# Kernel optimization log

Hardware: AMD Instinct MI355X
Metric: run time of the kernel (lower is better)

The kernel has to match this reference:

```python
import jax, jax.numpy as jnp
import numpy as np

B, N = 32, 25200          # batch, anchors (YOLOX @ 1280, strides 8/16/32)
NUM_CLASSES = 80
CH = 5 + NUM_CLASSES
CONF_THRE = 0.7
NMS_THRE = 0.45
TOPK = 512                # fixed pre-/post-NMS candidate budget (jit-static)
CLASS_OFFSET = 4096.0     # class-offset trick from the torch code


def setup_inputs() -> dict:
    key = jax.random.key(0)
    pred = jax.random.uniform(key, (B, N, CH), dtype=jnp.float32)
    # put box coords in pixel scale so IoU/NMS behaves realistically
    pred = pred.at[..., :4].multiply(640.0)
    return {"prediction": pred}


def _pairwise_iou(boxes):
    # boxes: [K, 4] xyxy -> iou: [K, K] (same math as torchvision.ops.nms)
    x1, y1, x2, y2 = boxes[:, 0], boxes[:, 1], boxes[:, 2], boxes[:, 3]
    area = (x2 - x1) * (y2 - y1)
    iw = jnp.clip(jnp.minimum(x2[:, None], x2[None, :]) - jnp.maximum(x1[:, None], x1[None, :]), 0.0)
    ih = jnp.clip(jnp.minimum(y2[:, None], y2[None, :]) - jnp.maximum(y1[:, None], y1[None, :]), 0.0)
    inter = iw * ih
    return inter / (area[:, None] + area[None, :] - inter)


def _greedy_nms(boxes, valid, iou_thre):
    # boxes are pre-sorted by descending score; greedy suppression identical to torchvision NMS
    iou = _pairwise_iou(boxes)  # [K, K]
    idx = jnp.arange(boxes.shape[0])

    def body(i, keep):
        suppress = (iou[i] > iou_thre) & (idx > i) & keep[i]
        return keep & ~suppress

    return jax.lax.fori_loop(0, boxes.shape[0], body, valid)


def _per_image(pred):
    # pred: [N, 5+C]
    cx, cy, w, h = pred[:, 0], pred[:, 1], pred[:, 2], pred[:, 3]
    hw, hh = w * 0.5, h * 0.5
    boxes = jnp.stack([cx - hw, cy - hh, cx + hw, cy + hh], axis=1)  # [N, 4] xyxy

    cls_scores = pred[:, 5:5 + NUM_CLASSES]
    class_conf = jnp.max(cls_scores, axis=1)
    class_pred = jnp.argmax(cls_scores, axis=1)
    conf = pred[:, 4] * class_conf                      # obj * class score
    valid = conf >= CONF_THRE

    # confidence filter + sort-by-score via fixed-size top-k (invalids ranked last)
    rank = jnp.where(valid, conf, -1.0)
    _, order = jax.lax.top_k(rank, TOPK)                # [TOPK], descending score
    b = boxes[order]
    c = conf[order]
    cl = class_pred[order]
    v = valid[order]

    nms_boxes = b + cl.astype(b.dtype)[:, None] * CLASS_OFFSET
    keep = _greedy_nms(nms_boxes, v, NMS_THRE)          # [TOPK] bool

    det = jnp.concatenate([b, c[:, None], cl.astype(jnp.float32)[:, None]], axis=1)  # [TOPK, 6]
    det = det * jax.lax.stop_gradient(keep.astype(det.dtype))[:, None]
    return det, keep


def reference(prediction):
    # returns padded detections [B, TOPK, 6] (x1,y1,x2,y2,conf,cls) and keep mask [B, TOPK]
    det, keep = jax.vmap(_per_image)(prediction)
    return det, keep
```

## Files before the change

kernel.cpp:

```cpp
#include <hip/hip_runtime.h>
#include <stdint.h>

#define BATCH 32
#define NANCH 25200
#define CH 85
#define NCLS 80
#define TOPK 512
#define CONF_THRE 0.7f
#define NMS_THRE 0.45f
#define CLS_OFF 4096.0f
#define NCHUNK 25
#define CHUNK 1008

typedef unsigned long long u64;
typedef unsigned int u32;

#define OFF_CONF  0
#define OFF_HIST  3225600
#define OFF_NMS   4044800
#define OFF_DET   4372480
#define OFF_VALID 4765696
#define OFF_MASK  4767744

__global__ __launch_bounds__(256) void scan_kernel(const float* __restrict__ pred,
                                                   u32* __restrict__ conf32) {
    const int tid = threadIdx.x;
    const int lane = tid & 63;
    const int wv = tid >> 6;
    const int g = lane >> 4;
    const int l = lane & 15;
    const int a = blockIdx.x * 16 + wv * 4 + g;
    const size_t base = (size_t)a * CH;

    float m = -1.0f, obj = 0.0f;
    {
        const float4 q = *(const float4*)(pred + base + (l << 2));
        const int p = l << 2;
        if (p + 0 >= 5) m = fmaxf(m, q.x); else if (p + 0 == 4) obj = q.x;
        if (p + 1 >= 5) m = fmaxf(m, q.y); else if (p + 1 == 4) obj = q.y;
        if (p + 2 >= 5) m = fmaxf(m, q.z); else if (p + 2 == 4) obj = q.z;
        if (p + 3 >= 5) m = fmaxf(m, q.w); else if (p + 3 == 4) obj = q.w;
    }
    if (l < 5) {
        const float4 q = *(const float4*)(pred + base + 64 + (l << 2));
        m = fmaxf(fmaxf(m, fmaxf(q.x, q.y)), fmaxf(q.z, q.w));
    } else if (l == 5) {
        m = fmaxf(m, pred[base + 84]);
    }
    #pragma unroll
    for (int off = 1; off < 16; off <<= 1) m = fmaxf(m, __shfl_xor(m, off));
    const float ob = __shfl(obj, (lane & 48) + 1);
    const float conf = ob * m;
    if (l == 0)
        conf32[a] = (conf >= CONF_THRE) ? __float_as_uint(conf) : 0u;
}

__global__ __launch_bounds__(256) void hist_kernel(const u32* __restrict__ conf32,
                                                   u32* __restrict__ histG) {
    __shared__ u32 h[256];
    const int img = blockIdx.x, chunk = blockIdx.y, tid = threadIdx.x;
    h[tid] = 0u;
    __syncthreads();
    const u32* cd = conf32 + (size_t)img * NANCH + chunk * CHUNK;
    for (int i = tid; i < CHUNK; i += 256) {
        const u32 c = cd[i];
        if (c) atomicAdd(&h[(c >> 15) & 255u], 1u);
    }
    __syncthreads();
    histG[((size_t)img * NCHUNK + chunk) * 256 + tid] = h[tid];
}

__global__ __launch_bounds__(1024) void select_kernel(const float* __restrict__ pred,
                                                      const u32* __restrict__ conf32,
                                                      const u32* __restrict__ histG,
                                                      float* __restrict__ nmsG,
                                                      float* __restrict__ detG,
                                                      u64* __restrict__ validG) {
    __shared__ u64 sbuf[1024];
    __shared__ u64 sorted[1024];
    __shared__ u32 hist[256];
    __shared__ u32 wtot[4];
    __shared__ u32 s_cnt, s_pivot;
    __shared__ unsigned char val[TOPK];

    const int img = blockIdx.x;
    const int tid = threadIdx.x;
    const int lane = tid & 63;
    const int wv = tid >> 6;

    if (tid == 0) { s_cnt = 0u; s_pivot = 0u; }
    if (tid < 256) {
        const u32* hsrc = histG + (size_t)img * (NCHUNK * 256) + tid;
        u32 s0 = 0;
        #pragma unroll
        for (int c = 0; c < NCHUNK; ++c) s0 += hsrc[c * 256];
        hist[tid] = s0;
    }
    __syncthreads();
    u32 v = 0, s = 0;
    if (tid < 256) {
        v = hist[tid]; s = v;
        #pragma unroll
        for (int off = 1; off < 64; off <<= 1) {
            const u32 t = __shfl_down(s, off);
            if (lane + off < 64) s += t;
        }
        if (lane == 0) wtot[wv] = s;
    }
    __syncthreads();
    if (tid < 256) {
        u32 add = 0;
        for (int w2 = wv + 1; w2 < 4; ++w2) add += wtot[w2];
        const u32 sfull = s + add;
        const u32 snext = sfull - v;
        if (sfull >= TOPK && snext < TOPK) s_pivot = (u32)tid;
    }
    __syncthreads();
    const u32 T = 0x3F000000u | (s_pivot << 15);

    const u32* cd = conf32 + (size_t)img * NANCH;
    for (int i = tid; i < NANCH; i += 1024) {
        const u32 c = cd[i];
        if (c >= T) {
            const u32 pos = atomicAdd(&s_cnt, 1u);
            if (pos < 1024u)
                sbuf[pos] = ((u64)c << 32) | (u64)(0xFFFFFFFFu - (u32)i);
        }
    }
    __syncthreads();
    const u32 mc = (s_cnt > 1024u) ? 1024u : s_cnt;

    sorted[tid] = 0ull;
    u32 rank = 0; u64 my = 0ull;
    if (tid < (int)mc) {
        my = sbuf[tid];
        for (u32 i = 0; i < mc; ++i) rank += (sbuf[i] > my) ? 1u : 0u;
    }
    __syncthreads();
    if (tid < (int)mc && rank < 1024u) sorted[rank] = my;
    __syncthreads();

    float* nb_ = nmsG + (size_t)img * (5 * TOPK);
    float* dt_ = detG + (size_t)img * (6 * TOPK);
    for (int r = wv; r < TOPK; r += 16) {
        const u64 key = sorted[r];
        const float conf = __uint_as_float((u32)(key >> 32));
        const bool okrow = conf >= CONF_THRE;
        float x1 = 0.f, y1 = 0.f, x2 = 0.f, y2 = 0.f, clsf = 0.f;
        if (okrow) {
            const u32 anchor = 0xFFFFFFFFu - (u32)(key & 0xFFFFFFFFull);
            const float* row = pred + ((size_t)img * NANCH + anchor) * CH;
            float vv = row[5 + lane];
            int ci = lane;
            if (lane < 16) {
                const float v2 = row[69 + lane];
                if (v2 > vv) { vv = v2; ci = 64 + lane; }
            }
            #pragma unroll
            for (int off = 32; off > 0; off >>= 1) {
                const float ov = __shfl_xor(vv, off);
                const int oi = __shfl_xor(ci, off);
                if (ov > vv || (ov == vv && oi < ci)) { vv = ov; ci = oi; }
            }
            const float cx = row[0], cy = row[1], w = row[2], h = row[3];
            const float hw = w * 0.5f, hh = h * 0.5f;
            x1 = cx - hw; y1 = cy - hh; x2 = cx + hw; y2 = cy + hh;
            clsf = (float)ci;
        }
        if (lane == 0) {
            const float off = clsf * CLS_OFF;
            const float X1 = x1 + off, Y1 = y1 + off, X2 = x2 + off, Y2 = y2 + off;
            nb_[0 * TOPK + r] = X1; nb_[1 * TOPK + r] = Y1;
            nb_[2 * TOPK + r] = X2; nb_[3 * TOPK + r] = Y2;
            nb_[4 * TOPK + r] = (X2 - X1) * (Y2 - Y1);
            dt_[r * 6 + 0] = x1; dt_[r * 6 + 1] = y1;
            dt_[r * 6 + 2] = x2; dt_[r * 6 + 3] = y2;
            dt_[r * 6 + 4] = okrow ? conf : 0.0f;
            dt_[r * 6 + 5] = clsf;
            val[r] = okrow ? 1 : 0;
        }
    }
    __syncthreads();

    if (tid < TOPK) {
        const u64 vb = __ballot(val[tid] != 0);
        if (lane == 0) validG[img * 8 + wv] = vb;
    }
}

__global__ __launch_bounds__(256) void iou_kernel(const float* __restrict__ nmsG,
                                                  u64* __restrict__ maskG) {
    __shared__ float bx1[TOPK], by1[TOPK], bx2[TOPK], by2[TOPK], bar[TOPK];
    const int img = blockIdx.x;
    const int slab = blockIdx.y;
    const int tid = threadIdx.x;
    const int lane = tid & 63;
    const float* nb_ = nmsG + (size_t)img * (5 * TOPK);
    for (int i = tid; i < TOPK; i += 256) {
        bx1[i] = nb_[i];            by1[i] = nb_[TOPK + i];
        bx2[i] = nb_[2 * TOPK + i]; by2[i] = nb_[3 * TOPK + i];
        bar[i] = nb_[4 * TOPK + i];
    }
    __syncthreads();
    const int q0 = slab * (16 * TOPK);
    for (int q = q0 + tid; q < q0 + 16 * TOPK; q += 256) {
        const int i = q >> 9;
        const int j = q & (TOPK - 1);
        bool sup = false;
        if (j > i) {
            const float xx1 = fmaxf(bx1[i], bx1[j]);
            const float yy1 = fmaxf(by1[i], by1[j]);
            const float xx2 = fminf(bx2[i], bx2[j]);
            const float yy2 = fminf(by2[i], by2[j]);
            const float iw = fmaxf(xx2 - xx1, 0.0f);
            const float ih = fmaxf(yy2 - yy1, 0.0f);
            const float inter = iw * ih;
            const float uni = bar[i] + bar[j] - inter;
            const float iou = inter / uni;
            sup = iou > NMS_THRE;
        }
        const u64 bm = __ballot(sup);
        if (lane == 0) maskG[(size_t)img * 4096 + (q >> 6)] = bm;
    }
}

__global__ __launch_bounds__(256) void greedy_kernel(const u64* __restrict__ maskG,
                                                     const u64* __restrict__ validG,
                                                     const float* __restrict__ detG,
                                                     float* __restrict__ out) {
    __shared__ u64 m[TOPK * 8];
    __shared__ u64 kw8[8];
    const int img = blockIdx.x;
    const int tid = threadIdx.x;
    const int lane = tid & 63;
    const int wv = tid >> 6;
    const u64* mg = maskG + (size_t)img * 4096;
    for (int i = tid; i < 4096; i += 256) m[i] = mg[i];
    __syncthreads();

    if (wv == 0) {
        const bool ld = lane < 8;
        u64 kw = ld ? validG[img * 8 + lane] : 0ull;
        u64 p0 = ld ? m[0 * 8 + lane] : 0ull;
        u64 p1 = ld ? m[1 * 8 + lane] : 0ull;
        u64 p2 = ld ? m[2 * 8 + lane] : 0ull;
        u64 p3 = ld ? m[3 * 8 + lane] : 0ull;
        for (int i = 0; i < TOPK; i += 4) {
            {
                const u64 w = __shfl(kw, i >> 6);
                const u64 bit = (w >> (i & 63)) & 1ull;
                kw &= ~(p0 & (0ull - bit));
                p0 = (ld && i + 4 < TOPK) ? m[(i + 4) * 8 + lane] : 0ull;
            }
            {
                const u64 w = __shfl(kw, (i + 1) >> 6);
                const u64 bit = (w >> ((i + 1) & 63)) & 1ull;
                kw &= ~(p1 & (0ull - bit));
                p1 = (ld && i + 5 < TOPK) ? m[(i + 5) * 8 + lane] : 0ull;
            }
            {
                const u64 w = __shfl(kw, (i + 2) >> 6);
                const u64 bit = (w >> ((i + 2) & 63)) & 1ull;
                kw &= ~(p2 & (0ull - bit));
                p2 = (ld && i + 6 < TOPK) ? m[(i + 6) * 8 + lane] : 0ull;
            }
            {
                const u64 w = __shfl(kw, (i + 3) >> 6);
                const u64 bit = (w >> ((i + 3) & 63)) & 1ull;
                kw &= ~(p3 & (0ull - bit));
                p3 = (ld && i + 7 < TOPK) ? m[(i + 7) * 8 + lane] : 0ull;
            }
        }
        if (ld) kw8[lane] = kw;
    }
    __syncthreads();

    const float* dt_ = detG + (size_t)img * (6 * TOPK);
    float* det_out = out + (size_t)img * (TOPK * 6);
    float* keep_out = out + (size_t)BATCH * TOPK * 6 + (size_t)img * TOPK;
    for (int idx = tid; idx < TOPK * 6; idx += 256) {
        const int r = idx / 6;
        const float kf = ((kw8[r >> 6] >> (r & 63)) & 1ull) ? 1.0f : 0.0f;
        det_out[idx] = dt_[idx] * kf;
    }
    for (int r = tid; r < TOPK; r += 256) {
        keep_out[r] = ((kw8[r >> 6] >> (r & 63)) & 1ull) ? 1.0f : 0.0f;
    }
}

extern "C" void kernel_launch(void* const* d_in, const int* in_sizes, int n_in,
                              void* d_out, int out_size, void* d_ws, size_t ws_size,
                              hipStream_t stream) {
    const float* pred = (const float*)d_in[0];
    float* out = (float*)d_out;
    char* ws = (char*)d_ws;
    u32* conf32 = (u32*)(ws + OFF_CONF);
    u32* histG = (u32*)(ws + OFF_HIST);
    float* nmsG = (float*)(ws + OFF_NMS);
    float* detG = (float*)(ws + OFF_DET);
    u64* validG = (u64*)(ws + OFF_VALID);
    u64* maskG = (u64*)(ws + OFF_MASK);

    scan_kernel<<<(BATCH * NANCH) / 16, 256, 0, stream>>>(pred, conf32);
    dim3 g2(BATCH, NCHUNK);
    hist_kernel<<<g2, 256, 0, stream>>>(conf32, histG);
    select_kernel<<<BATCH, 1024, 0, stream>>>(pred, conf32, histG, nmsG, detG, validG);
    dim3 g4(BATCH, 32);
    iou_kernel<<<g4, 256, 0, stream>>>(nmsG, maskG);
    greedy_kernel<<<BATCH, 256, 0, stream>>>(maskG, validG, detG, out);
}
```

Measured before the change: 484.2 us.

## Fuse histogram into scan and merge select, IoU and greedy into one kernel

Builds the per-image score histogram with global atomics inside the scan kernel, after a small zeroing kernel, so the separate histogram pass is gone. The select, IoU-mask and greedy NMS stages are merged into one 1024-thread block per image that keeps boxes, the suppression mask and detections in shared memory instead of writing them to global memory. The goal is fewer launches and less global round-tripping. In exchange, the IoU matrix is computed by only 32 blocks rather than 1024, and global atomics may contend on the histogram bins.

```diff
diff --git a/kernel.cpp b/kernel.cpp
--- a/kernel.cpp
+++ b/kernel.cpp
@@ -9,21 +9,20 @@
 #define CONF_THRE 0.7f
 #define NMS_THRE 0.45f
 #define CLS_OFF 4096.0f
-#define NCHUNK 25
-#define CHUNK 1008
 
 typedef unsigned long long u64;
 typedef unsigned int u32;
 
-#define OFF_CONF  0
-#define OFF_HIST  3225600
-#define OFF_NMS   4044800
-#define OFF_DET   4372480
-#define OFF_VALID 4765696
-#define OFF_MASK  4767744
+#define OFF_CONF 0
+#define OFF_HIST 3225600
+
+__global__ __launch_bounds__(256) void zero_kernel(u32* __restrict__ histG) {
+    histG[blockIdx.x * 256 + threadIdx.x] = 0u;
+}
 
 __global__ __launch_bounds__(256) void scan_kernel(const float* __restrict__ pred,
-                                                   u32* __restrict__ conf32) {
+                                                   u32* __restrict__ conf32,
+                                                   u32* __restrict__ histG) {
     const int tid = threadIdx.x;
     const int lane = tid & 63;
     const int wv = tid >> 6;
@@ -51,37 +50,31 @@
     for (int off = 1; off < 16; off <<= 1) m = fmaxf(m, __shfl_xor(m, off));
     const float ob = __shfl(obj, (lane & 48) + 1);
     const float conf = ob * m;
-    if (l == 0)
-        conf32[a] = (conf >= CONF_THRE) ? __float_as_uint(conf) : 0u;
+    if (l == 0) {
+        const bool ok = conf >= CONF_THRE;
+        const u32 c = __float_as_uint(conf);
+        conf32[a] = ok ? c : 0u;
+        if (ok) {
+            const int img = a / NANCH;
+            atomicAdd(&histG[img * 256 + ((c >> 15) & 255u)], 1u);
+        }
+    }
 }
 
-__global__ __launch_bounds__(256) void hist_kernel(const u32* __restrict__ conf32,
-                                                   u32* __restrict__ histG) {
-    __shared__ u32 h[256];
-    const int img = blockIdx.x, chunk = blockIdx.y, tid = threadIdx.x;
-    h[tid] = 0u;
-    __syncthreads();
-    const u32* cd = conf32 + (size_t)img * NANCH + chunk * CHUNK;
-    for (int i = tid; i < CHUNK; i += 256) {
-        const u32 c = cd[i];
-        if (c) atomicAdd(&h[(c >> 15) & 255u], 1u);
-    }
-    __syncthreads();
-    histG[((size_t)img * NCHUNK + chunk) * 256 + tid] = h[tid];
-}
-
-__global__ __launch_bounds__(1024) void select_kernel(const float* __restrict__ pred,
-                                                      const u32* __restrict__ conf32,
-                                                      const u32* __restrict__ histG,
-                                                      float* __restrict__ nmsG,
-                                                      float* __restrict__ detG,
-                                                      u64* __restrict__ validG) {
+__global__ __launch_bounds__(1024) void mega_kernel(const float* __restrict__ pred,
+                                                    const u32* __restrict__ conf32,
+                                                    const u32* __restrict__ histG,
+                                                    float* __restrict__ out) {
     __shared__ u64 sbuf[1024];
     __shared__ u64 sorted[1024];
-    __shared__ u32 hist[256];
+    __shared__ u64 smask[TOPK * 8];
+    __shared__ float sdet[TOPK * 6];
+    __shared__ float bx1[TOPK], by1[TOPK], bx2[TOPK], by2[TOPK], bar[TOPK];
+    __shared__ unsigned char val[TOPK];
     __shared__ u32 wtot[4];
     __shared__ u32 s_cnt, s_pivot;
-    __shared__ unsigned char val[TOPK];
+    __shared__ u64 kwinit[8];
+    __shared__ u64 kw8[8];
 
     const int img = blockIdx.x;
     const int tid = threadIdx.x;
@@ -89,17 +82,11 @@
     const int wv = tid >> 6;
 
     if (tid == 0) { s_cnt = 0u; s_pivot = 0u; }
-    if (tid < 256) {
-        const u32* hsrc = histG + (size_t)img * (NCHUNK * 256) + tid;
-        u32 s0 = 0;
-        #pragma unroll
-        for (int c = 0; c < NCHUNK; ++c) s0 += hsrc[c * 256];
-        hist[tid] = s0;
-    }
-    __syncthreads();
+
     u32 v = 0, s = 0;
     if (tid < 256) {
-        v = hist[tid]; s = v;
+        v = histG[(size_t)img * 256 + tid];
+        s = v;
         #pragma unroll
         for (int off = 1; off < 64; off <<= 1) {
             const u32 t = __shfl_down(s, off);
@@ -140,151 +127,166 @@
     if (tid < (int)mc && rank < 1024u) sorted[rank] = my;
     __syncthreads();
 
-    float* nb_ = nmsG + (size_t)img * (5 * TOPK);
-    float* dt_ = detG + (size_t)img * (6 * TOPK);
-    for (int r = wv; r < TOPK; r += 16) {
-        const u64 key = sorted[r];
-        const float conf = __uint_as_float((u32)(key >> 32));
-        const bool okrow = conf >= CONF_THRE;
-        float x1 = 0.f, y1 = 0.f, x2 = 0.f, y2 = 0.f, clsf = 0.f;
-        if (okrow) {
-            const u32 anchor = 0xFFFFFFFFu - (u32)(key & 0xFFFFFFFFull);
+    for (int r0 = wv; r0 < 256; r0 += 16) {
+        const int rA = r0, rB = r0 + 256;
+        const u64 keyA = sorted[rA];
+        const u64 keyB = sorted[rB];
+        const float confA = __uint_as_float((u32)(keyA >> 32));
+        const float confB = __uint_as_float((u32)(keyB >> 32));
+        const bool okA = confA >= CONF_THRE;
+        const bool okB = confB >= CONF_THRE;
+        float vA = -1.0f, vB = -1.0f;
+        float cxA = 0.f, cyA = 0.f, wwA = 0.f, hhA = 0.f;
+        float cxB = 0.f, cyB = 0.f, wwB = 0.f, hhB = 0.f;
+        int ciA = lane, ciB = lane;
+        if (okA) {
+            const u32 anchor = 0xFFFFFFFFu - (u32)(keyA & 0xFFFFFFFFull);
             const float* row = pred + ((size_t)img * NANCH + anchor) * CH;
-            float vv = row[5 + lane];
-            int ci = lane;
+            vA = row[5 + lane];
             if (lane < 16) {
                 const float v2 = row[69 + lane];
-                if (v2 > vv) { vv = v2; ci = 64 + lane; }
-            }
-            #pragma unroll
-            for (int off = 32; off > 0; off >>= 1) {
-                const float ov = __shfl_xor(vv, off);
-                const int oi = __shfl_xor(ci, off);
-                if (ov > vv || (ov == vv && oi < ci)) { vv = ov; ci = oi; }
-            }
-            const float cx = row[0], cy = row[1], w = row[2], h = row[3];
-            const float hw = w * 0.5f, hh = h * 0.5f;
-            x1 = cx - hw; y1 = cy - hh; x2 = cx + hw; y2 = cy + hh;
-            clsf = (float)ci;
+                if (v2 > vA) { vA = v2; ciA = 64 + lane; }
+            }
+            if (lane == 0) { cxA = row[0]; cyA = row[1]; wwA = row[2]; hhA = row[3]; }
+        }
+        if (okB) {
+            const u32 anchor = 0xFFFFFFFFu - (u32)(keyB & 0xFFFFFFFFull);
+            const float* row = pred + ((size_t)img * NANCH + anchor) * CH;
+            vB = row[5 + lane];
+            if (lane < 16) {
+                const float v2 = row[69 + lane];
+                if (v2 > vB) { vB = v2; ciB = 64 + lane; }
+            }
+            if (lane == 0) { cxB = row[0]; cyB = row[1]; wwB = row[2]; hhB = row[3]; }
+        }
+        #pragma unroll
+        for (int off = 32; off > 0; off >>= 1) {
+            const float ov = __shfl_xor(vA, off);
+            const int oi = __shfl_xor(ciA, off);
+            if (ov > vA || (ov == vA && oi < ciA)) { vA = ov; ciA = oi; }
+        }
+        #pragma unroll
+        for (int off = 32; off > 0; off >>= 1) {
+            const float ov = __shfl_xor(vB, off);
+            const int oi = __shfl_xor(ciB, off);
+            if (ov > vB || (ov == vB && oi < ciB)) { vB = ov; ciB = oi; }
         }
         if (lane == 0) {
-            const float off = clsf * CLS_OFF;
-            const float X1 = x1 + off, Y1 = y1 + off, X2 = x2 + off, Y2 = y2 + off;
-            nb_[0 * TOPK + r] = X1; nb_[1 * TOPK + r] = Y1;
-            nb_[2 * TOPK + r] = X2; nb_[3 * TOPK + r] = Y2;
-            nb_[4 * TOPK + r] = (X2 - X1) * (Y2 - Y1);
-            dt_[r * 6 + 0] = x1; dt_[r * 6 + 1] = y1;
-            dt_[r * 6 + 2] = x2; dt_[r * 6 + 3] = y2;
-            dt_[r * 6 + 4] = okrow ? conf : 0.0f;
-            dt_[r * 6 + 5] = clsf;
-            val[r] = okrow ? 1 : 0;
+            {
+                const float clsf = okA ? (float)ciA : 0.0f;
+                const float hw = wwA * 0.5f, hh = hhA * 0.5f;
+                const float x1 = cxA - hw, y1 = cyA - hh, x2 = cxA + hw, y2 = cyA + hh;
+                const float off = clsf * CLS_OFF;
+                const float X1 = x1 + off, Y1 = y1 + off, X2 = x2 + off, Y2 = y2 + off;
+                bx1[rA] = X1; by1[rA] = Y1; bx2[rA] = X2; by2[rA] = Y2;
+                bar[rA] = (X2 - X1) * (Y2 - Y1);
+                sdet[rA * 6 + 0] = x1; sdet[rA * 6 + 1] = y1;
+                sdet[rA * 6 + 2] = x2; sdet[rA * 6 + 3] = y2;
+                sdet[rA * 6 + 4] = okA ? confA : 0.0f;
+                sdet[rA * 6 + 5] = clsf;
+                val[rA] = okA ? 1 : 0;
+            }
+            {
+                const float clsf = okB ? (float)ciB : 0.0f;
+                const float hw = wwB * 0.5f, hh = hhB * 0.5f;
+                const float x1 = cxB - hw, y1 = cyB - hh, x2 = cxB + hw, y2 = cyB + hh;
+                const float off = clsf * CLS_OFF;
+                const float X1 = x1 + off, Y1 = y1 + off, X2 = x2 + off, Y2 = y2 + off;
+                bx1[rB] = X1; by1[rB] = Y1; bx2[rB] = X2; by2[rB] = Y2;
+                bar[rB] = (X2 - X1) * (Y2 - Y1);
+                sdet[rB * 6 + 0] = x1; sdet[rB * 6 + 1] = y1;
+                sdet[rB * 6 + 2] = x2; sdet[rB * 6 + 3] = y2;
+                sdet[rB * 6 + 4] = okB ? confB : 0.0f;
+                sdet[rB * 6 + 5] = clsf;
+                val[rB] = okB ? 1 : 0;
+            }
         }
     }
     __syncthreads();
 
     if (tid < TOPK) {
         const u64 vb = __ballot(val[tid] != 0);
-        if (lane == 0) validG[img * 8 + wv] = vb;
-    }
-}
-
-__global__ __launch_bounds__(256) void iou_kernel(const float* __restrict__ nmsG,
-                                                  u64* __restrict__ maskG) {
-    __shared__ float bx1[TOPK], by1[TOPK], bx2[TOPK], by2[TOPK], bar[TOPK];
-    const int img = blockIdx.x;
-    const int slab = blockIdx.y;
-    const int tid = threadIdx.x;
-    const int lane = tid & 63;
-    const float* nb_ = nmsG + (size_t)img * (5 * TOPK);
-    for (int i = tid; i < TOPK; i += 256) {
-        bx1[i] = nb_[i];            by1[i] = nb_[TOPK + i];
-        bx2[i] = nb_[2 * TOPK + i]; by2[i] = nb_[3 * TOPK + i];
-        bar[i] = nb_[4 * TOPK + i];
-    }
-    __syncthreads();
-    const int q0 = slab * (16 * TOPK);
-    for (int q = q0 + tid; q < q0 + 16 * TOPK; q += 256) {
-        const int i = q >> 9;
-        const int j = q & (TOPK - 1);
-        bool sup = false;
-        if (j > i) {
-            const float xx1 = fmaxf(bx1[i], bx1[j]);
-            const float yy1 = fmaxf(by1[i], by1[j]);
-            const float xx2 = fminf(bx2[i], bx2[j]);
-            const float yy2 = fminf(by2[i], by2[j]);
-            const float iw = fmaxf(xx2 - xx1, 0.0f);
-            const float ih = fmaxf(yy2 - yy1, 0.0f);
-            const float inter = iw * ih;
-            const float uni = bar[i] + bar[j] - inter;
-            const float iou = inter / uni;
-            sup = iou > NMS_THRE;
-        }
-        const u64 bm = __ballot(sup);
-        if (lane == 0) maskG[(size_t)img * 4096 + (q >> 6)] = bm;
-    }
-}
-
-__global__ __launch_bounds__(256) void greedy_kernel(const u64* __restrict__ maskG,
-                                                     const u64* __restrict__ validG,
-                                                     const float* __restrict__ detG,
-                                                     float* __restrict__ out) {
-    __shared__ u64 m[TOPK * 8];
-    __shared__ u64 kw8[8];
-    const int img = blockIdx.x;
-    const int tid = threadIdx.x;
-    const int lane = tid & 63;
-    const int wv = tid >> 6;
-    const u64* mg = maskG + (size_t)img * 4096;
-    for (int i = tid; i < 4096; i += 256) m[i] = mg[i];
+        if (lane == 0) kwinit[wv] = vb;
+    }
+
+    float jx1[8], jy1[8], jx2[8], jy2[8], jar[8];
+    #pragma unroll
+    for (int jb = 0; jb < 8; ++jb) {
+        const int j = jb * 64 + lane;
+        jx1[jb] = bx1[j]; jy1[jb] = by1[j];
+        jx2[jb] = bx2[j]; jy2[jb] = by2[j];
+        jar[jb] = bar[j];
+    }
+    for (int i = wv * 32; i < wv * 32 + 32; ++i) {
+        const float ix1 = bx1[i], iy1 = by1[i], ix2 = bx2[i], iy2 = by2[i], iar = bar[i];
+        #pragma unroll
+        for (int jb = 0; jb < 8; ++jb) {
+            const int j = jb * 64 + lane;
+            bool sup = false;
+            if (j > i) {
+                const float xx1 = fmaxf(ix1, jx1[jb]);
+                const float yy1 = fmaxf(iy1, jy1[jb]);
+                const float xx2 = fminf(ix2, jx2[jb]);
+                const float yy2 = fminf(iy2, jy2[jb]);
+                const float iw = fmaxf(xx2 - xx1, 0.0f);
+                const float ih = fmaxf(yy2 - yy1, 0.0f);
+                const float inter = iw * ih;
+                const float uni = iar + jar[jb] - inter;
+                const float iou = inter / uni;
+                sup = iou > NMS_THRE;
+            }
+            const u64 bm = __ballot(sup);
+            if (lane == 0) smask[i * 8 + jb] = bm;
+        }
+    }
     __syncthreads();
 
     if (wv == 0) {
         const bool ld = lane < 8;
-        u64 kw = ld ? validG[img * 8 + lane] : 0ull;
-        u64 p0 = ld ? m[0 * 8 + lane] : 0ull;
-        u64 p1 = ld ? m[1 * 8 + lane] : 0ull;
-        u64 p2 = ld ? m[2 * 8 + lane] : 0ull;
-        u64 p3 = ld ? m[3 * 8 + lane] : 0ull;
+        u64 kw = ld ? kwinit[lane] : 0ull;
+        u64 p0 = ld ? smask[0 * 8 + lane] : 0ull;
+        u64 p1 = ld ? smask[1 * 8 + lane] : 0ull;
+        u64 p2 = ld ? smask[2 * 8 + lane] : 0ull;
+        u64 p3 = ld ? smask[3 * 8 + lane] : 0ull;
         for (int i = 0; i < TOPK; i += 4) {
             {
                 const u64 w = __shfl(kw, i >> 6);
                 const u64 bit = (w >> (i & 63)) & 1ull;
                 kw &= ~(p0 & (0ull - bit));
-                p0 = (ld && i + 4 < TOPK) ? m[(i + 4) * 8 + lane] : 0ull;
+                p0 = (ld && i + 4 < TOPK) ? smask[(i + 4) * 8 + lane] : 0ull;
             }
             {
                 const u64 w = __shfl(kw, (i + 1) >> 6);
                 const u64 bit = (w >> ((i + 1) & 63)) & 1ull;
                 kw &= ~(p1 & (0ull - bit));
-                p1 = (ld && i + 5 < TOPK) ? m[(i + 5) * 8 + lane] : 0ull;
+                p1 = (ld && i + 5 < TOPK) ? smask[(i + 5) * 8 + lane] : 0ull;
             }
             {
                 const u64 w = __shfl(kw, (i + 2) >> 6);
                 const u64 bit = (w >> ((i + 2) & 63)) & 1ull;
                 kw &= ~(p2 & (0ull - bit));
-                p2 = (ld && i + 6 < TOPK) ? m[(i + 6) * 8 + lane] : 0ull;
+                p2 = (ld && i + 6 < TOPK) ? smask[(i + 6) * 8 + lane] : 0ull;
             }
             {
                 const u64 w = __shfl(kw, (i + 3) >> 6);
                 const u64 bit = (w >> ((i + 3) & 63)) & 1ull;
                 kw &= ~(p3 & (0ull - bit));
-                p3 = (ld && i + 7 < TOPK) ? m[(i + 7) * 8 + lane] : 0ull;
+                p3 = (ld && i + 7 < TOPK) ? smask[(i + 7) * 8 + lane] : 0ull;
             }
         }
         if (ld) kw8[lane] = kw;
     }
     __syncthreads();
 
-    const float* dt_ = detG + (size_t)img * (6 * TOPK);
     float* det_out = out + (size_t)img * (TOPK * 6);
     float* keep_out = out + (size_t)BATCH * TOPK * 6 + (size_t)img * TOPK;
-    for (int idx = tid; idx < TOPK * 6; idx += 256) {
+    for (int idx = tid; idx < TOPK * 6; idx += 1024) {
         const int r = idx / 6;
         const float kf = ((kw8[r >> 6] >> (r & 63)) & 1ull) ? 1.0f : 0.0f;
-        det_out[idx] = dt_[idx] * kf;
-    }
-    for (int r = tid; r < TOPK; r += 256) {
-        keep_out[r] = ((kw8[r >> 6] >> (r & 63)) & 1ull) ? 1.0f : 0.0f;
+        det_out[idx] = sdet[idx] * kf;
+    }
+    if (tid < TOPK) {
+        keep_out[tid] = ((kw8[tid >> 6] >> (tid & 63)) & 1ull) ? 1.0f : 0.0f;
     }
 }
 
@@ -296,16 +298,8 @@
     char* ws = (char*)d_ws;
     u32* conf32 = (u32*)(ws + OFF_CONF);
     u32* histG = (u32*)(ws + OFF_HIST);
-    float* nmsG = (float*)(ws + OFF_NMS);
-    float* detG = (float*)(ws + OFF_DET);
-    u64* validG = (u64*)(ws + OFF_VALID);
-    u64* maskG = (u64*)(ws + OFF_MASK);
-
-    scan_kernel<<<(BATCH * NANCH) / 16, 256, 0, stream>>>(pred, conf32);
-    dim3 g2(BATCH, NCHUNK);
-    hist_kernel<<<g2, 256, 0, stream>>>(conf32, histG);
-    select_kernel<<<BATCH, 1024, 0, stream>>>(pred, conf32, histG, nmsG, detG, validG);
-    dim3 g4(BATCH, 32);
-    iou_kernel<<<g4, 256, 0, stream>>>(nmsG, maskG);
-    greedy_kernel<<<BATCH, 256, 0, stream>>>(maskG, validG, detG, out);
+
+    zero_kernel<<<BATCH, 256, 0, stream>>>(histG);
+    scan_kernel<<<(BATCH * NANCH) / 16, 256, 0, stream>>>(pred, conf32, histG);
+    mega_kernel<<<BATCH, 1024, 0, stream>>>(pred, conf32, histG, out);
 }
```

Result: slower. 527.4 us (+8.9%).
